# Optimization experiments

Hardware: AMD Instinct MI355X
Metric: run time of the kernel (lower is better)

## Reference

```python
import jax, jax.numpy as jnp
import numpy as np

M, K, N = 8192, 4096, 12288


def setup_inputs() -> dict:
    key = jax.random.key(0)
    k1, k2, k3, k4 = jax.random.split(key, 4)
    input_tensor = jax.random.normal(k1, (1, M, K), dtype=jnp.float32)
    # int8 quantized weight [N, K] and per-output-channel scale [N, 1]
    weight = jax.random.randint(k2, (N, K), -127, 128, dtype=jnp.int32).astype(jnp.int8)
    weight_scale = (jax.random.uniform(k3, (N, 1), dtype=jnp.float32) * 0.01 + 1e-4)
    bias = jax.random.normal(k4, (N,), dtype=jnp.float32) * 0.1
    return {"input_tensor": input_tensor, "weight": weight,
            "weight_scale": weight_scale, "bias": bias}


def reference(input_tensor, weight, weight_scale, bias):
    x = input_tensor[0]  # squeeze(0) -> [M, K]
    # dynamic per-token symmetric int8 quantization: scale = absmax/127
    a_scale = jnp.max(jnp.abs(x), axis=-1, keepdims=True) / 127.0  # [M, 1]
    q = jnp.clip(jnp.round(x / a_scale), -128.0, 127.0)  # int8 values held in f32
    # int8 GEMM accumulated (emulated in f32), then dequant with per-token x per-channel scales
    acc = jnp.einsum('mk,nk->mn', q, weight.astype(jnp.float32))  # [M, N]
    out = acc * a_scale * weight_scale[:, 0][None, :] + bias[None, :]
    return out[None].astype(input_tensor.dtype)  # unsqueeze(0) -> [1, M, N]
```

## Files before the change

### kernel.cpp

```cpp
#include <hip/hip_runtime.h>
#include <cstdint>

#define M_DIM 8192
#define K_DIM 4096
#define N_DIM 12288

#define BM 128
#define BN 128
#define BK 128

using i32x4 = __attribute__((ext_vector_type(4))) int;

__device__ inline void gload_lds16(const void* g, void* l) {
    __builtin_amdgcn_global_load_lds(
        (const __attribute__((address_space(1))) void*)g,
        (__attribute__((address_space(3))) void*)l,
        16, 0, 0);
}

__global__ __launch_bounds__(256) void pack_w(const int* __restrict__ w32,
                                              int8_t* __restrict__ wq) {
    const size_t total4 = (size_t)N_DIM * K_DIM / 4;
    const size_t stride = (size_t)gridDim.x * blockDim.x;
    int* out32 = (int*)wq;
    for (size_t i = (size_t)blockIdx.x * blockDim.x + threadIdx.x; i < total4;
         i += stride) {
        const int4 v = ((const int4*)w32)[i];
        out32[i] = (v.x & 255) | ((v.y & 255) << 8) | ((v.z & 255) << 16) | (v.w << 24);
    }
}

__global__ __launch_bounds__(256) void quant_rows(const float* __restrict__ x,
                                                  int8_t* __restrict__ qa,
                                                  float* __restrict__ ascale) {
    const int row = blockIdx.x;
    const int t = threadIdx.x;
    const float4* xr = (const float4*)(x + (size_t)row * K_DIM);
    float4 v[4];
    float amax = 0.0f;
#pragma unroll
    for (int c = 0; c < 4; ++c) {
        v[c] = xr[t + 256 * c];
        amax = fmaxf(amax, fmaxf(fmaxf(fabsf(v[c].x), fabsf(v[c].y)),
                                 fmaxf(fabsf(v[c].z), fabsf(v[c].w))));
    }
#pragma unroll
    for (int off = 32; off > 0; off >>= 1)
        amax = fmaxf(amax, __shfl_xor(amax, off));
    __shared__ float smax[4];
    if ((t & 63) == 0) smax[t >> 6] = amax;
    __syncthreads();
    amax = fmaxf(fmaxf(smax[0], smax[1]), fmaxf(smax[2], smax[3]));
    const float sc = amax * (1.0f / 127.0f);
    const float inv = (amax > 0.0f) ? (127.0f / amax) : 0.0f;
    if (t == 0) ascale[row] = sc;

    int* q32 = (int*)(qa + (size_t)row * K_DIM);
#pragma unroll
    for (int c = 0; c < 4; ++c) {
        int q0 = (int)rintf(v[c].x * inv);
        int q1 = (int)rintf(v[c].y * inv);
        int q2 = (int)rintf(v[c].z * inv);
        int q3 = (int)rintf(v[c].w * inv);
        q0 = min(127, max(-128, q0));
        q1 = min(127, max(-128, q1));
        q2 = min(127, max(-128, q2));
        q3 = min(127, max(-128, q3));
        q32[t + 256 * c] = (q0 & 255) | ((q1 & 255) << 8) | ((q2 & 255) << 16) | (q3 << 24);
    }
}

__global__ __launch_bounds__(256) void gemm_i8(const int8_t* __restrict__ qa,
                                               const int8_t* __restrict__ w,
                                               const float* __restrict__ ascale,
                                               const float* __restrict__ wscale,
                                               const float* __restrict__ bias,
                                               float* __restrict__ out) {
    __shared__ int8_t lA[BM * BK];
    __shared__ int8_t lB[BN * BK];

    const int t = threadIdx.x;
    const int bn = blockIdx.x;
    const int bm = blockIdx.y;
    const int lane = t & 63;
    const int wave = t >> 6;
    const int wm = wave >> 1;
    const int wn = wave & 1;
    const int lrow = lane & 15;
    const int lk = lane >> 4;
    const int swz = lrow & 7;

    const int srow = t >> 3;
    const int pslot = t & 7;
    const int kslot = pslot ^ (srow & 7);

    const size_t a_base = (size_t)(bm * BM + srow) * K_DIM + (size_t)kslot * 16;
    const size_t b_base = (size_t)(bn * BN + srow) * K_DIM + (size_t)kslot * 16;

    i32x4 acc[4][4] = {};

    for (int kt = 0; kt < K_DIM / BK; ++kt) {
        const size_t koff = (size_t)kt * BK;
#pragma unroll
        for (int i = 0; i < 4; ++i)
            gload_lds16(qa + a_base + koff + (size_t)(32 * i) * K_DIM,
                        &lA[t * 16 + i * 4096]);
#pragma unroll
        for (int i = 0; i < 4; ++i)
            gload_lds16(w + b_base + koff + (size_t)(32 * i) * K_DIM,
                        &lB[t * 16 + i * 4096]);
        __syncthreads();

#pragma unroll
        for (int kh = 0; kh < 2; ++kh) {
            i32x4 af[4], bf[4];
#pragma unroll
            for (int m = 0; m < 4; ++m) {
                const int r = wm * 64 + m * 16 + lrow;
                af[m] = *(const i32x4*)&lA[r * BK + (((kh * 4 + lk) ^ swz) << 4)];
            }
#pragma unroll
            for (int n = 0; n < 4; ++n) {
                const int r = wn * 64 + n * 16 + lrow;
                bf[n] = *(const i32x4*)&lB[r * BK + (((kh * 4 + lk) ^ swz) << 4)];
            }
#pragma unroll
            for (int m = 0; m < 4; ++m)
#pragma unroll
                for (int n = 0; n < 4; ++n)
                    acc[m][n] = __builtin_amdgcn_mfma_i32_16x16x64_i8(
                        af[m], bf[n], acc[m][n], 0, 0, 0);
        }
        __syncthreads();
    }

    const int r0 = bm * BM + wm * 64;
    const int c0 = bn * BN + wn * 64;
    float asc[4][4];
#pragma unroll
    for (int m = 0; m < 4; ++m)
#pragma unroll
        for (int j = 0; j < 4; ++j)
            asc[m][j] = ascale[r0 + m * 16 + lk * 4 + j];
#pragma unroll
    for (int n = 0; n < 4; ++n) {
        const int col = c0 + n * 16 + lrow;
        const float wsc = wscale[col];
        const float bb = bias[col];
#pragma unroll
        for (int m = 0; m < 4; ++m) {
#pragma unroll
            for (int j = 0; j < 4; ++j) {
                const int row = r0 + m * 16 + lk * 4 + j;
                out[(size_t)row * N_DIM + col] = (float)acc[m][n][j] * asc[m][j] * wsc + bb;
            }
        }
    }
}

extern "C" void kernel_launch(void* const* d_in, const int* in_sizes, int n_in,
                              void* d_out, int out_size, void* d_ws, size_t ws_size,
                              hipStream_t stream) {
    const float* x = (const float*)d_in[0];
    const int* w32 = (const int*)d_in[1];
    const float* wscale = (const float*)d_in[2];
    const float* bias = (const float*)d_in[3];
    float* out = (float*)d_out;

    int8_t* qa = (int8_t*)d_ws;
    float* ascale = (float*)((char*)d_ws + (size_t)M_DIM * K_DIM);
    int8_t* wq = (int8_t*)((char*)d_ws + (size_t)M_DIM * K_DIM +
                           (size_t)M_DIM * sizeof(float));

    pack_w<<<2048, 256, 0, stream>>>(w32, wq);
    quant_rows<<<M_DIM, 256, 0, stream>>>(x, qa, ascale);
    gemm_i8<<<dim3(N_DIM / BN, M_DIM / BM), 256, 0, stream>>>(qa, wq, ascale, wscale,
                                                              bias, out);
}
```

Measured before the change: 624.3 us.

## Fuse quant/pack kernels and pipeline GEMM with 256x256 tiles and 4-stage LDS ring

Merges the activation quantization and weight packing into one launch, removing a kernel launch boundary. Rewrites the int8 GEMM to use 256x256 output tiles with 512 threads, BK=64, and a 4-buffer LDS ring. Global-to-LDS loads are prefetched two tiles ahead, using explicit vmcnt waits and a single barrier per iteration. Also adds grouped block swizzling for L2 locality and raises wave priority around the MFMA burst. The larger tile increases register pressure (32 accumulators) and uses 128KB of LDS per block, which may limit occupancy.

```diff
diff --git a/kernel.cpp b/kernel.cpp
--- a/kernel.cpp
+++ b/kernel.cpp
@@ -4,10 +4,7 @@
 #define M_DIM 8192
 #define K_DIM 4096
 #define N_DIM 12288
-
-#define BM 128
-#define BN 128
-#define BK 128
+#define KTILES (K_DIM / 64)
 
 using i32x4 = __attribute__((ext_vector_type(4))) int;
 
@@ -18,127 +15,147 @@
         16, 0, 0);
 }
 
-__global__ __launch_bounds__(256) void pack_w(const int* __restrict__ w32,
-                                              int8_t* __restrict__ wq) {
-    const size_t total4 = (size_t)N_DIM * K_DIM / 4;
-    const size_t stride = (size_t)gridDim.x * blockDim.x;
-    int* out32 = (int*)wq;
-    for (size_t i = (size_t)blockIdx.x * blockDim.x + threadIdx.x; i < total4;
-         i += stride) {
-        const int4 v = ((const int4*)w32)[i];
-        out32[i] = (v.x & 255) | ((v.y & 255) << 8) | ((v.z & 255) << 16) | (v.w << 24);
+__global__ __launch_bounds__(256) void quant_pack(const float* __restrict__ x,
+                                                  const int* __restrict__ w32,
+                                                  int8_t* __restrict__ qa,
+                                                  float* __restrict__ ascale,
+                                                  int8_t* __restrict__ wq) {
+    const int t = threadIdx.x;
+    if (blockIdx.x < M_DIM) {
+        const int row = blockIdx.x;
+        const float4* xr = (const float4*)(x + (size_t)row * K_DIM);
+        float4 v[4];
+        float amax = 0.0f;
+#pragma unroll
+        for (int c = 0; c < 4; ++c) {
+            v[c] = xr[t + 256 * c];
+            amax = fmaxf(amax, fmaxf(fmaxf(fabsf(v[c].x), fabsf(v[c].y)),
+                                     fmaxf(fabsf(v[c].z), fabsf(v[c].w))));
+        }
+#pragma unroll
+        for (int off = 32; off > 0; off >>= 1)
+            amax = fmaxf(amax, __shfl_xor(amax, off));
+        __shared__ float smax[4];
+        if ((t & 63) == 0) smax[t >> 6] = amax;
+        __syncthreads();
+        amax = fmaxf(fmaxf(smax[0], smax[1]), fmaxf(smax[2], smax[3]));
+        const float sc = amax * (1.0f / 127.0f);
+        const float inv = (amax > 0.0f) ? (127.0f / amax) : 0.0f;
+        if (t == 0) ascale[row] = sc;
+
+        int* q32 = (int*)(qa + (size_t)row * K_DIM);
+#pragma unroll
+        for (int c = 0; c < 4; ++c) {
+            int q0 = (int)rintf(v[c].x * inv);
+            int q1 = (int)rintf(v[c].y * inv);
+            int q2 = (int)rintf(v[c].z * inv);
+            int q3 = (int)rintf(v[c].w * inv);
+            q0 = min(127, max(-128, q0));
+            q1 = min(127, max(-128, q1));
+            q2 = min(127, max(-128, q2));
+            q3 = min(127, max(-128, q3));
+            q32[t + 256 * c] = (q0 & 255) | ((q1 & 255) << 8) | ((q2 & 255) << 16) | (q3 << 24);
+        }
+    } else {
+        const int pb = blockIdx.x - M_DIM;
+        const size_t total4 = (size_t)N_DIM * K_DIM / 4;
+        const size_t stride = (size_t)2048 * 256;
+        int* out32 = (int*)wq;
+        for (size_t i = (size_t)pb * 256 + t; i < total4; i += stride) {
+            const int4 v = ((const int4*)w32)[i];
+            out32[i] = (v.x & 255) | ((v.y & 255) << 8) | ((v.z & 255) << 16) | (v.w << 24);
+        }
     }
 }
 
-__global__ __launch_bounds__(256) void quant_rows(const float* __restrict__ x,
-                                                  int8_t* __restrict__ qa,
-                                                  float* __restrict__ ascale) {
-    const int row = blockIdx.x;
-    const int t = threadIdx.x;
-    const float4* xr = (const float4*)(x + (size_t)row * K_DIM);
-    float4 v[4];
-    float amax = 0.0f;
-#pragma unroll
-    for (int c = 0; c < 4; ++c) {
-        v[c] = xr[t + 256 * c];
-        amax = fmaxf(amax, fmaxf(fmaxf(fabsf(v[c].x), fabsf(v[c].y)),
-                                 fmaxf(fabsf(v[c].z), fabsf(v[c].w))));
-    }
-#pragma unroll
-    for (int off = 32; off > 0; off >>= 1)
-        amax = fmaxf(amax, __shfl_xor(amax, off));
-    __shared__ float smax[4];
-    if ((t & 63) == 0) smax[t >> 6] = amax;
-    __syncthreads();
-    amax = fmaxf(fmaxf(smax[0], smax[1]), fmaxf(smax[2], smax[3]));
-    const float sc = amax * (1.0f / 127.0f);
-    const float inv = (amax > 0.0f) ? (127.0f / amax) : 0.0f;
-    if (t == 0) ascale[row] = sc;
-
-    int* q32 = (int*)(qa + (size_t)row * K_DIM);
-#pragma unroll
-    for (int c = 0; c < 4; ++c) {
-        int q0 = (int)rintf(v[c].x * inv);
-        int q1 = (int)rintf(v[c].y * inv);
-        int q2 = (int)rintf(v[c].z * inv);
-        int q3 = (int)rintf(v[c].w * inv);
-        q0 = min(127, max(-128, q0));
-        q1 = min(127, max(-128, q1));
-        q2 = min(127, max(-128, q2));
-        q3 = min(127, max(-128, q3));
-        q32[t + 256 * c] = (q0 & 255) | ((q1 & 255) << 8) | ((q2 & 255) << 16) | (q3 << 24);
-    }
-}
-
-__global__ __launch_bounds__(256) void gemm_i8(const int8_t* __restrict__ qa,
-                                               const int8_t* __restrict__ w,
-                                               const float* __restrict__ ascale,
-                                               const float* __restrict__ wscale,
-                                               const float* __restrict__ bias,
-                                               float* __restrict__ out) {
-    __shared__ int8_t lA[BM * BK];
-    __shared__ int8_t lB[BN * BK];
+__global__ __launch_bounds__(512, 2) void gemm_i8(const int8_t* __restrict__ qa,
+                                                  const int8_t* __restrict__ wq,
+                                                  const float* __restrict__ ascale,
+                                                  const float* __restrict__ wscale,
+                                                  const float* __restrict__ bias,
+                                                  float* __restrict__ out) {
+    __shared__ int8_t lds[4][2][256 * 64];
 
     const int t = threadIdx.x;
-    const int bn = blockIdx.x;
-    const int bm = blockIdx.y;
     const int lane = t & 63;
     const int wave = t >> 6;
-    const int wm = wave >> 1;
-    const int wn = wave & 1;
+    const int wm = wave >> 2;
+    const int wn = wave & 3;
     const int lrow = lane & 15;
     const int lk = lane >> 4;
-    const int swz = lrow & 7;
+    const int elr = ((lrow ^ (lrow >> 2)) & 3);
 
-    const int srow = t >> 3;
-    const int pslot = t & 7;
-    const int kslot = pslot ^ (srow & 7);
+    const int flat = blockIdx.x;
+    const int sw = (flat & 7) * 192 + (flat >> 3);
+    const int bm = sw / 48;
+    const int bn = sw % 48;
 
-    const size_t a_base = (size_t)(bm * BM + srow) * K_DIM + (size_t)kslot * 16;
-    const size_t b_base = (size_t)(bn * BN + srow) * K_DIM + (size_t)kslot * 16;
+    const int rA0 = t >> 2;
+    const int rA1 = (t >> 2) + 128;
+    const int kA0 = (t & 3) ^ ((rA0 ^ (rA0 >> 2)) & 3);
+    const int kA1 = (t & 3) ^ ((rA1 ^ (rA1 >> 2)) & 3);
+    const size_t aoff0 = (size_t)(bm * 256 + rA0) * K_DIM + (size_t)kA0 * 16;
+    const size_t aoff1 = (size_t)(bm * 256 + rA1) * K_DIM + (size_t)kA1 * 16;
+    const size_t boff0 = (size_t)(bn * 256 + rA0) * K_DIM + (size_t)kA0 * 16;
+    const size_t boff1 = (size_t)(bn * 256 + rA1) * K_DIM + (size_t)kA1 * 16;
 
-    i32x4 acc[4][4] = {};
-
-    for (int kt = 0; kt < K_DIM / BK; ++kt) {
-        const size_t koff = (size_t)kt * BK;
-#pragma unroll
-        for (int i = 0; i < 4; ++i)
-            gload_lds16(qa + a_base + koff + (size_t)(32 * i) * K_DIM,
-                        &lA[t * 16 + i * 4096]);
-#pragma unroll
-        for (int i = 0; i < 4; ++i)
-            gload_lds16(w + b_base + koff + (size_t)(32 * i) * K_DIM,
-                        &lB[t * 16 + i * 4096]);
-        __syncthreads();
+    i32x4 acc[8][4] = {};
 
 #pragma unroll
-        for (int kh = 0; kh < 2; ++kh) {
-            i32x4 af[4], bf[4];
-#pragma unroll
-            for (int m = 0; m < 4; ++m) {
-                const int r = wm * 64 + m * 16 + lrow;
-                af[m] = *(const i32x4*)&lA[r * BK + (((kh * 4 + lk) ^ swz) << 4)];
-            }
-#pragma unroll
-            for (int n = 0; n < 4; ++n) {
-                const int r = wn * 64 + n * 16 + lrow;
-                bf[n] = *(const i32x4*)&lB[r * BK + (((kh * 4 + lk) ^ swz) << 4)];
-            }
-#pragma unroll
-            for (int m = 0; m < 4; ++m)
-#pragma unroll
-                for (int n = 0; n < 4; ++n)
-                    acc[m][n] = __builtin_amdgcn_mfma_i32_16x16x64_i8(
-                        af[m], bf[n], acc[m][n], 0, 0, 0);
-        }
-        __syncthreads();
+    for (int p = 0; p < 2; ++p) {
+        const size_t ko = (size_t)p * 64;
+        gload_lds16(qa + aoff0 + ko, &lds[p][0][t * 16]);
+        gload_lds16(qa + aoff1 + ko, &lds[p][0][t * 16 + 8192]);
+        gload_lds16(wq + boff0 + ko, &lds[p][1][t * 16]);
+        gload_lds16(wq + boff1 + ko, &lds[p][1][t * 16 + 8192]);
     }
 
-    const int r0 = bm * BM + wm * 64;
-    const int c0 = bn * BN + wn * 64;
-    float asc[4][4];
+    for (int j = 0; j < KTILES; ++j) {
+        const int cb = j & 3;
+        if (j + 2 < KTILES) {
+            const int sb = (j + 2) & 3;
+            const size_t ko = (size_t)(j + 2) * 64;
+            gload_lds16(qa + aoff0 + ko, &lds[sb][0][t * 16]);
+            gload_lds16(qa + aoff1 + ko, &lds[sb][0][t * 16 + 8192]);
+            gload_lds16(wq + boff0 + ko, &lds[sb][1][t * 16]);
+            gload_lds16(wq + boff1 + ko, &lds[sb][1][t * 16 + 8192]);
+            asm volatile("s_waitcnt vmcnt(8)" ::: "memory");
+        } else if (j + 1 < KTILES) {
+            asm volatile("s_waitcnt vmcnt(4)" ::: "memory");
+        } else {
+            asm volatile("s_waitcnt vmcnt(0)" ::: "memory");
+        }
+        __builtin_amdgcn_s_barrier();
+        __builtin_amdgcn_sched_barrier(0);
+
+        const int8_t* __restrict__ LA = lds[cb][0];
+        const int8_t* __restrict__ LB = lds[cb][1];
+        i32x4 af[8], bf[4];
 #pragma unroll
-    for (int m = 0; m < 4; ++m)
+        for (int m = 0; m < 8; ++m) {
+            const int r = wm * 128 + m * 16 + lrow;
+            af[m] = *(const i32x4*)&LA[r * 64 + ((lk ^ elr) << 4)];
+        }
+#pragma unroll
+        for (int n = 0; n < 4; ++n) {
+            const int r = wn * 64 + n * 16 + lrow;
+            bf[n] = *(const i32x4*)&LB[r * 64 + ((lk ^ elr) << 4)];
+        }
+        __builtin_amdgcn_s_setprio(1);
+#pragma unroll
+        for (int m = 0; m < 8; ++m)
+#pragma unroll
+            for (int n = 0; n < 4; ++n)
+                acc[m][n] = __builtin_amdgcn_mfma_i32_16x16x64_i8(af[m], bf[n],
+                                                                  acc[m][n], 0, 0, 0);
+        __builtin_amdgcn_s_setprio(0);
+    }
+
+    const int r0 = bm * 256 + wm * 128;
+    const int c0 = bn * 256 + wn * 64;
+    float asc[8][4];
+#pragma unroll
+    for (int m = 0; m < 8; ++m)
 #pragma unroll
         for (int j = 0; j < 4; ++j)
             asc[m][j] = ascale[r0 + m * 16 + lk * 4 + j];
@@ -148,7 +165,7 @@
         const float wsc = wscale[col];
         const float bb = bias[col];
 #pragma unroll
-        for (int m = 0; m < 4; ++m) {
+        for (int m = 0; m < 8; ++m) {
 #pragma unroll
             for (int j = 0; j < 4; ++j) {
                 const int row = r0 + m * 16 + lk * 4 + j;
@@ -172,8 +189,6 @@
     int8_t* wq = (int8_t*)((char*)d_ws + (size_t)M_DIM * K_DIM +
                            (size_t)M_DIM * sizeof(float));
 
-    pack_w<<<2048, 256, 0, stream>>>(w32, wq);
-    quant_rows<<<M_DIM, 256, 0, stream>>>(x, qa, ascale);
-    gemm_i8<<<dim3(N_DIM / BN, M_DIM / BM), 256, 0, stream>>>(qa, wq, ascale, wscale,
-                                                              bias, out);
+    quant_pack<<<M_DIM + 2048, 256, 0, stream>>>(x, w32, qa, ascale, wq);
+    gemm_i8<<<1536, 512, 0, stream>>>(qa, wq, ascale, wscale, bias, out);
 }
```

Result: faster. 543.4 us (-13.0%).
